# Kernel optimization log

Hardware: AMD Instinct MI355X
Metric: run time of the kernel (lower is better)

The kernel has to match this reference:

```python
import jax, jax.numpy as jnp
from jax import lax
import numpy as np

B, C, H, W = 16, 192, 128, 128
NF = 192


def hard_sigmoid(x):
    # Keras 1.x hard_sigmoid: clip(0.2*x + 0.5, 0, 1)
    return jnp.clip(0.2 * x + 0.5, 0.0, 1.0)


def setup_inputs() -> dict:
    key = jax.random.key(0)
    k1, k2, k3 = jax.random.split(key, 3)
    x = jax.random.normal(k1, (B, C, H, W), dtype=jnp.float32)
    W_iof = jax.random.normal(k2, (4 * NF, C, 1, 1), dtype=jnp.float32) * 0.05
    U_iof = jax.random.normal(k3, (4 * NF, NF, 3, 1), dtype=jnp.float32) * 0.05
    b_iof = jnp.zeros((4 * NF,), dtype=jnp.float32)
    init_h = jnp.zeros((NF, W), dtype=jnp.float32)
    init_c = jnp.zeros((NF, W), dtype=jnp.float32)
    return {"x": x, "W_iof": W_iof, "U_iof": U_iof, "b_iof": b_iof,
            "init_h": init_h, "init_c": init_c}


def reference(x, W_iof, U_iof, b_iof, init_h, init_c):
    b, c, h_dim, w_dim = x.shape
    nf = init_h.shape[0]
    in3 = c // 3
    out3 = nf // 3
    # pyramid channel mask on the 1x1 input-to-state weights
    mask = jnp.ones((4 * nf, c), dtype=x.dtype)
    mask = mask.at[:out3, in3:].set(0.0)
    mask = mask.at[out3:2 * out3, 2 * in3:].set(0.0)
    Wm = W_iof[:, :, 0, 0] * mask  # (4nf, c)
    U = U_iof[:, :, :, 0]          # (4nf, nf, 3)

    # direction 'Down': scan over rows (H). Precompute input-to-state for all rows.
    X = jnp.transpose(x, (0, 2, 1, 3))  # (B, H, C, W)
    i2s = jnp.einsum('bhcw,oc->bhow', X, Wm) + b_iof[None, None, :, None]  # (B,H,4nf,W)

    h0 = jnp.broadcast_to(init_h[None], (b, nf, w_dim))
    c0 = jnp.broadcast_to(init_c[None], (b, nf, w_dim))

    def step(carry, its):
        h_tm1, c_tm1 = carry
        # 3-wide cross-correlation along W, 'half' padding (lax conv is correlation)
        s2s = lax.conv_general_dilated(h_tm1, U, (1,), [(1, 1)],
                                       dimension_numbers=('NCH', 'OIH', 'NCH'))
        gates = its + s2s  # (B, 4nf, W)
        ofi = hard_sigmoid(gates[:, :3 * nf])
        o = ofi[:, :nf]
        f = ofi[:, nf:2 * nf]
        i = ofi[:, 2 * nf:3 * nf]
        g = jnp.tanh(gates[:, 3 * nf:])
        c_new = f * c_tm1 + i * g
        h_new = o * jnp.tanh(c_new)
        return (h_new, c_new), h_new

    _, hs = lax.scan(step, (h0, c0), jnp.transpose(i2s, (1, 0, 2, 3)))  # (H,B,nf,W)
    # return_sequences=True then permute (0,2,1,3): (B, H, nf, W) -> (B, nf, H, W)
    return jnp.transpose(hs, (1, 2, 0, 3))
```

## Files before the change

kernel.cpp:

```cpp
#include <hip/hip_runtime.h>
#include <math.h>

#define BB 16
#define CC 192
#define NF 192
#define HH 128
#define WW 128
#define G4 768
#define KTOT 768
#define LDA 776
#define NJB 12
#define GRIDSZ (NJB * BB)
#define SMEM_BYTES (64 * LDA * 2)

typedef __bf16 bf16x8 __attribute__((ext_vector_type(8)));
typedef float  f32x4  __attribute__((ext_vector_type(4)));

__device__ unsigned g_cnt[BB * 64];

__device__ __forceinline__ float hsig(float v) {
    float y = fmaf(0.2f, v, 0.5f);
    return fminf(fmaxf(y, 0.f), 1.f);
}

__device__ __forceinline__ float tanh_fast(float x) {
    float y = fminf(fmaxf(x, -8.f), 8.f) * 2.885390082f;
    float e = __builtin_amdgcn_exp2f(y);
    float r = __builtin_amdgcn_rcpf(e + 1.f);
    return fmaf(-2.f, r, 1.f);
}

__device__ __forceinline__ unsigned short f2bf(float f) {
    unsigned int u = __float_as_uint(f);
    u += 0x7fffu + ((u >> 16) & 1u);
    return (unsigned short)(u >> 16);
}

__global__ void prep_weights(const float* __restrict__ Wf,
                             const float* __restrict__ Uf,
                             unsigned short* __restrict__ Wc) {
    int idx = blockIdx.x * blockDim.x + threadIdx.x;
    if (idx < BB)
        g_cnt[idx * 64] = 0u;
    if (idx >= G4 * KTOT) return;
    int row = idx / KTOT;
    int k   = idx - row * KTOT;
    float v;
    if (k < CC) {
        int lim = row < 64 ? 64 : (row < 128 ? 128 : 192);
        v = (k < lim) ? Wf[row * CC + k] : 0.f;
    } else {
        int kp = k - CC;
        int d  = kp / CC;
        int c  = kp - d * CC;
        v = Uf[((size_t)row * CC + c) * 3 + d];
    }
    Wc[idx] = f2bf(v);
}

__global__ void prep_bx(const float* __restrict__ x, unsigned short* __restrict__ Bsrc) {
    int idx = blockIdx.x * blockDim.x + threadIdx.x;
    if (idx >= HH * BB * WW) return;
    int w = idx & (WW - 1);
    int r = idx >> 7;
    int b = r & (BB - 1);
    int t = r >> 4;
    const float* xp = x + ((size_t)b * CC * HH + t) * WW + w;
    unsigned short* dp = Bsrc + (size_t)idx * KTOT;
#pragma unroll
    for (int cc = 0; cc < CC / 8; ++cc) {
        unsigned short v[8];
#pragma unroll
        for (int i = 0; i < 8; ++i)
            v[i] = f2bf(xp[(size_t)(cc * 8 + i) * (HH * WW)]);
        *(uint4*)(dp + cc * 8) = *(uint4*)v;
    }
}

__global__ void prep_bh_oob(unsigned short* __restrict__ Bsrc) {
    int idx = blockIdx.x * blockDim.x + threadIdx.x;
    if (idx >= HH * BB * 384) return;
    int u = idx % 384;
    int r = idx / 384;
    int b = r & (BB - 1);
    int t = r >> 4;
    size_t base = ((size_t)(t * BB + b) * WW) * KTOT;
    size_t off = (u < 192) ? (size_t)0 * KTOT + 192 + u
                           : (size_t)127 * KTOT + 384 + u;
    Bsrc[base + off] = 0;
}

__global__ void prep_bh0(const float* __restrict__ init_h, unsigned short* __restrict__ Bsrc) {
    int idx = blockIdx.x * blockDim.x + threadIdx.x;
    if (idx >= BB * WW * 576) return;
    int kp = idx % 576;
    int r  = idx / 576;
    int w  = r & (WW - 1);
    int b  = r >> 7;
    int d  = kp / CC;
    int c  = kp - d * CC;
    int wt = w + d - 1;
    float v = (wt >= 0 && wt < WW) ? init_h[c * WW + wt] : 0.f;
    Bsrc[((size_t)b * WW + w) * KTOT + CC + kp] = f2bf(v);
}

__global__ __launch_bounds__(512, 1) void lstm_persist(
    const unsigned short* __restrict__ Wc,
    unsigned short* __restrict__ Bsrc,
    const float* __restrict__ bias,
    const float* __restrict__ init_c,
    float* __restrict__ out)
{
    extern __shared__ unsigned short smem[];
    unsigned short (*Alds)[LDA] = (unsigned short(*)[LDA])smem;

    const int tid  = threadIdx.x;
    const int nw   = tid >> 6;
    const int lane = tid & 63;
    const int m    = lane & 15;
    const int q    = lane >> 4;
    const int jb   = blockIdx.x % NJB;
    const int b    = blockIdx.x / NJB;
    const int j0   = jb * 16;
    const int w    = nw * 16 + m;
    unsigned* const cntp = &g_cnt[b * 64];

    for (int u = tid; u < 64 * 96; u += 512) {
        int r  = u / 96;
        int ko = (u - r * 96) * 8;
        int grow = (r >> 4) * NF + j0 + (r & 15);
        *(uint4*)&Alds[r][ko] = *(const uint4*)(Wc + (size_t)grow * KTOT + ko);
    }
    float breg[4][4];
#pragma unroll
    for (int g = 0; g < 4; ++g)
#pragma unroll
        for (int r = 0; r < 4; ++r)
            breg[g][r] = bias[g * NF + j0 + q * 4 + r];
    float creg[4];
#pragma unroll
    for (int r = 0; r < 4; ++r)
        creg[r] = init_c[(j0 + q * 4 + r) * WW + w];
    __syncthreads();

    bf16x8 bxc[6], bxn[6];
    {
        const unsigned short* B0 = Bsrc + ((size_t)b * WW + w) * KTOT;
#pragma unroll
        for (int kc = 0; kc < 6; ++kc)
            bxc[kc] = *(const bf16x8*)(B0 + kc * 32 + q * 8);
    }

    for (int t = 0; t < HH; ++t) {
        f32x4 acc[4];
#pragma unroll
        for (int g = 0; g < 4; ++g)
            acc[g] = (f32x4){breg[g][0], breg[g][1], breg[g][2], breg[g][3]};

        const unsigned short* Bn =
            Bsrc + ((size_t)(t * BB + b) * WW + w) * KTOT;

#pragma unroll
        for (int kc = 0; kc < 6; ++kc) {
            const int k = kc * 32 + q * 8;
            bf16x8 a0 = *(const bf16x8*)&Alds[ 0 + m][k];
            bf16x8 a1 = *(const bf16x8*)&Alds[16 + m][k];
            bf16x8 a2 = *(const bf16x8*)&Alds[32 + m][k];
            bf16x8 a3 = *(const bf16x8*)&Alds[48 + m][k];
            acc[0] = __builtin_amdgcn_mfma_f32_16x16x32_bf16(a0, bxc[kc], acc[0], 0, 0, 0);
            acc[1] = __builtin_amdgcn_mfma_f32_16x16x32_bf16(a1, bxc[kc], acc[1], 0, 0, 0);
            acc[2] = __builtin_amdgcn_mfma_f32_16x16x32_bf16(a2, bxc[kc], acc[2], 0, 0, 0);
            acc[3] = __builtin_amdgcn_mfma_f32_16x16x32_bf16(a3, bxc[kc], acc[3], 0, 0, 0);
        }

        if (t > 0) {
            const unsigned need = (unsigned)(NJB * t);
            while (__hip_atomic_load(cntp, __ATOMIC_RELAXED,
                                     __HIP_MEMORY_SCOPE_AGENT) < need)
                __builtin_amdgcn_s_sleep(1);
            __builtin_amdgcn_fence(__ATOMIC_ACQUIRE, "workgroup");
        }

        bf16x8 bh[18];
#pragma unroll
        for (int kc = 0; kc < 18; ++kc)
            bh[kc] = *(const bf16x8*)(Bn + 192 + kc * 32 + q * 8);

        if (t < HH - 1) {
            const unsigned short* Bx = Bn + (size_t)BB * WW * KTOT;
#pragma unroll
            for (int kc = 0; kc < 6; ++kc)
                bxn[kc] = *(const bf16x8*)(Bx + kc * 32 + q * 8);
        }

#pragma unroll
        for (int kc = 0; kc < 18; ++kc) {
            const int k = 192 + kc * 32 + q * 8;
            bf16x8 a0 = *(const bf16x8*)&Alds[ 0 + m][k];
            bf16x8 a1 = *(const bf16x8*)&Alds[16 + m][k];
            bf16x8 a2 = *(const bf16x8*)&Alds[32 + m][k];
            bf16x8 a3 = *(const bf16x8*)&Alds[48 + m][k];
            acc[0] = __builtin_amdgcn_mfma_f32_16x16x32_bf16(a0, bh[kc], acc[0], 0, 0, 0);
            acc[1] = __builtin_amdgcn_mfma_f32_16x16x32_bf16(a1, bh[kc], acc[1], 0, 0, 0);
            acc[2] = __builtin_amdgcn_mfma_f32_16x16x32_bf16(a2, bh[kc], acc[2], 0, 0, 0);
            acc[3] = __builtin_amdgcn_mfma_f32_16x16x32_bf16(a3, bh[kc], acc[3], 0, 0, 0);
        }

        float hn[4];
#pragma unroll
        for (int r = 0; r < 4; ++r) {
            float og = hsig(acc[0][r]);
            float fg = hsig(acc[1][r]);
            float ig = hsig(acc[2][r]);
            float gg = tanh_fast(acc[3][r]);
            float cn = fmaf(fg, creg[r], ig * gg);
            creg[r] = cn;
            hn[r] = og * tanh_fast(cn);
        }

        if (t < HH - 1) {
            unsigned long long pk =
                  (unsigned long long)f2bf(hn[0])
                | ((unsigned long long)f2bf(hn[1]) << 16)
                | ((unsigned long long)f2bf(hn[2]) << 32)
                | ((unsigned long long)f2bf(hn[3]) << 48);
            unsigned short* Bns =
                Bsrc + ((size_t)((t + 1) * BB + b) * WW) * KTOT;
            const int jo = CC + j0 + q * 4;
            __hip_atomic_store((unsigned long long*)
                (Bns + (size_t)w * KTOT + jo + CC), pk,
                __ATOMIC_RELAXED, __HIP_MEMORY_SCOPE_AGENT);
            if (w < WW - 1)
                __hip_atomic_store((unsigned long long*)
                    (Bns + (size_t)(w + 1) * KTOT + jo), pk,
                    __ATOMIC_RELAXED, __HIP_MEMORY_SCOPE_AGENT);
            if (w > 0)
                __hip_atomic_store((unsigned long long*)
                    (Bns + (size_t)(w - 1) * KTOT + jo + 2 * CC), pk,
                    __ATOMIC_RELAXED, __HIP_MEMORY_SCOPE_AGENT);
            asm volatile("s_waitcnt vmcnt(0)" ::: "memory");
            __syncthreads();
            if (tid == 0)
                __hip_atomic_fetch_add(cntp, 1u, __ATOMIC_RELAXED,
                                       __HIP_MEMORY_SCOPE_AGENT);
        }

#pragma unroll
        for (int r = 0; r < 4; ++r)
            out[(((size_t)b * NF + j0 + q * 4 + r) * HH + t) * WW + w] = hn[r];

#pragma unroll
        for (int kc = 0; kc < 6; ++kc)
            bxc[kc] = bxn[kc];
    }
}

extern "C" void kernel_launch(void* const* d_in, const int* in_sizes, int n_in,
                              void* d_out, int out_size, void* d_ws, size_t ws_size,
                              hipStream_t stream) {
    const float* x      = (const float*)d_in[0];
    const float* W_iof  = (const float*)d_in[1];
    const float* U_iof  = (const float*)d_in[2];
    const float* b_iof  = (const float*)d_in[3];
    const float* init_h = (const float*)d_in[4];
    const float* init_c = (const float*)d_in[5];
    float* out = (float*)d_out;

    unsigned short* Wc   = (unsigned short*)d_ws;
    unsigned short* Bsrc = Wc + (size_t)G4 * KTOT;

    prep_weights<<<(G4 * KTOT + 255) / 256, 256, 0, stream>>>(W_iof, U_iof, Wc);
    prep_bx<<<(HH * BB * WW + 255) / 256, 256, 0, stream>>>(x, Bsrc);
    prep_bh_oob<<<(HH * BB * 384 + 255) / 256, 256, 0, stream>>>(Bsrc);
    prep_bh0<<<(BB * WW * 576 + 255) / 256, 256, 0, stream>>>(init_h, Bsrc);

    const unsigned short* Wcp = Wc;
    unsigned short* Bsp = Bsrc;
    const float* bp = b_iof;
    const float* icp = init_c;
    float* op = out;
    void* args[] = {&Wcp, &Bsp, &bp, &icp, &op};
    hipLaunchCooperativeKernel((const void*)lstm_persist, dim3(GRIDSZ), dim3(512),
                               args, SMEM_BYTES, stream);
}
```

Before: 1.459 ms.

## Switch to 32x32x16 MFMA with split-K across two wave groups and LDS reduction

```diff
diff --git a/kernel.cpp b/kernel.cpp
--- a/kernel.cpp
+++ b/kernel.cpp
@@ -11,10 +11,12 @@
 #define LDA 776
 #define NJB 12
 #define GRIDSZ (NJB * BB)
-#define SMEM_BYTES (64 * LDA * 2)
+#define RED_STRIDE 36
+#define SMEM_BYTES (64 * LDA * 2 + 4 * 64 * RED_STRIDE * 4)
 
 typedef __bf16 bf16x8 __attribute__((ext_vector_type(8)));
 typedef float  f32x4  __attribute__((ext_vector_type(4)));
+typedef float  f32x16 __attribute__((ext_vector_type(16)));
 
 __device__ unsigned g_cnt[BB * 64];
 
@@ -113,16 +115,19 @@
 {
     extern __shared__ unsigned short smem[];
     unsigned short (*Alds)[LDA] = (unsigned short(*)[LDA])smem;
+    float* red = (float*)(smem + 64 * LDA);
 
     const int tid  = threadIdx.x;
     const int nw   = tid >> 6;
     const int lane = tid & 63;
-    const int m    = lane & 15;
-    const int q    = lane >> 4;
+    const int c31  = lane & 31;
+    const int l5   = lane >> 5;
+    const bool grp0 = (nw < 4);
+    const int ws   = grp0 ? nw : nw - 4;
+    const int w    = ws * 32 + c31;
     const int jb   = blockIdx.x % NJB;
     const int b    = blockIdx.x / NJB;
     const int j0   = jb * 16;
-    const int w    = nw * 16 + m;
     unsigned* const cntp = &g_cnt[b * 64];
 
     for (int u = tid; u < 64 * 96; u += 512) {
@@ -131,46 +136,55 @@
         int grow = (r >> 4) * NF + j0 + (r & 15);
         *(uint4*)&Alds[r][ko] = *(const uint4*)(Wc + (size_t)grow * KTOT + ko);
     }
-    float breg[4][4];
-#pragma unroll
-    for (int g = 0; g < 4; ++g)
-#pragma unroll
-        for (int r = 0; r < 4; ++r)
-            breg[g][r] = bias[g * NF + j0 + q * 4 + r];
-    float creg[4];
-#pragma unroll
-    for (int r = 0; r < 4; ++r)
-        creg[r] = init_c[(j0 + q * 4 + r) * WW + w];
+
+    float biasr[4][8];
+    float creg[8];
+    if (grp0) {
+#pragma unroll
+        for (int r = 0; r < 8; ++r) {
+            const int jq = (r & 3) + 8 * (r >> 2) + 4 * l5;
+#pragma unroll
+            for (int g = 0; g < 4; ++g)
+                biasr[g][r] = bias[g * NF + j0 + jq];
+            creg[r] = init_c[(j0 + jq) * WW + w];
+        }
+    }
     __syncthreads();
 
-    bf16x8 bxc[6], bxn[6];
-    {
+    bf16x8 bxc[12], bxn[12];
+    if (grp0) {
         const unsigned short* B0 = Bsrc + ((size_t)b * WW + w) * KTOT;
 #pragma unroll
-        for (int kc = 0; kc < 6; ++kc)
-            bxc[kc] = *(const bf16x8*)(B0 + kc * 32 + q * 8);
-    }
-
+        for (int s = 0; s < 12; ++s)
+            bxc[s] = *(const bf16x8*)(B0 + s * 16 + l5 * 8);
+    }
+
+    float hn[8];
     for (int t = 0; t < HH; ++t) {
-        f32x4 acc[4];
-#pragma unroll
-        for (int g = 0; g < 4; ++g)
-            acc[g] = (f32x4){breg[g][0], breg[g][1], breg[g][2], breg[g][3]};
+        f32x16 acc0, acc1;
+        if (grp0) {
+#pragma unroll
+            for (int r = 0; r < 8; ++r) {
+                acc0[r] = biasr[0][r]; acc0[r + 8] = biasr[1][r];
+                acc1[r] = biasr[2][r]; acc1[r + 8] = biasr[3][r];
+            }
+        } else {
+#pragma unroll
+            for (int i = 0; i < 16; ++i) { acc0[i] = 0.f; acc1[i] = 0.f; }
+        }
 
         const unsigned short* Bn =
             Bsrc + ((size_t)(t * BB + b) * WW + w) * KTOT;
 
-#pragma unroll
-        for (int kc = 0; kc < 6; ++kc) {
-            const int k = kc * 32 + q * 8;
-            bf16x8 a0 = *(const bf16x8*)&Alds[ 0 + m][k];
-            bf16x8 a1 = *(const bf16x8*)&Alds[16 + m][k];
-            bf16x8 a2 = *(const bf16x8*)&Alds[32 + m][k];
-            bf16x8 a3 = *(const bf16x8*)&Alds[48 + m][k];
-            acc[0] = __builtin_amdgcn_mfma_f32_16x16x32_bf16(a0, bxc[kc], acc[0], 0, 0, 0);
-            acc[1] = __builtin_amdgcn_mfma_f32_16x16x32_bf16(a1, bxc[kc], acc[1], 0, 0, 0);
-            acc[2] = __builtin_amdgcn_mfma_f32_16x16x32_bf16(a2, bxc[kc], acc[2], 0, 0, 0);
-            acc[3] = __builtin_amdgcn_mfma_f32_16x16x32_bf16(a3, bxc[kc], acc[3], 0, 0, 0);
+        if (grp0) {
+#pragma unroll
+            for (int s = 0; s < 12; ++s) {
+                const int k = s * 16 + l5 * 8;
+                bf16x8 a0 = *(const bf16x8*)&Alds[c31][k];
+                bf16x8 a1 = *(const bf16x8*)&Alds[32 + c31][k];
+                acc0 = __builtin_amdgcn_mfma_f32_32x32x16_bf16(a0, bxc[s], acc0, 0, 0, 0);
+                acc1 = __builtin_amdgcn_mfma_f32_32x32x16_bf16(a1, bxc[s], acc1, 0, 0, 0);
+            }
         }
 
         if (t > 0) {
@@ -181,77 +195,130 @@
             __builtin_amdgcn_fence(__ATOMIC_ACQUIRE, "workgroup");
         }
 
-        bf16x8 bh[18];
-#pragma unroll
-        for (int kc = 0; kc < 18; ++kc)
-            bh[kc] = *(const bf16x8*)(Bn + 192 + kc * 32 + q * 8);
+        if (grp0) {
+            bf16x8 bd[12];
+#pragma unroll
+            for (int s = 0; s < 12; ++s)
+                bd[s] = *(const bf16x8*)(Bn + 192 + s * 16 + l5 * 8);
+            if (t < HH - 1) {
+                const unsigned short* Bx = Bn + (size_t)BB * WW * KTOT;
+#pragma unroll
+                for (int s = 0; s < 12; ++s)
+                    bxn[s] = *(const bf16x8*)(Bx + s * 16 + l5 * 8);
+            }
+#pragma unroll
+            for (int s = 0; s < 12; ++s) {
+                const int k = (12 + s) * 16 + l5 * 8;
+                bf16x8 a0 = *(const bf16x8*)&Alds[c31][k];
+                bf16x8 a1 = *(const bf16x8*)&Alds[32 + c31][k];
+                acc0 = __builtin_amdgcn_mfma_f32_32x32x16_bf16(a0, bd[s], acc0, 0, 0, 0);
+                acc1 = __builtin_amdgcn_mfma_f32_32x32x16_bf16(a1, bd[s], acc1, 0, 0, 0);
+            }
+        } else {
+            bf16x8 bh[24];
+#pragma unroll
+            for (int s = 0; s < 24; ++s)
+                bh[s] = *(const bf16x8*)(Bn + 384 + s * 16 + l5 * 8);
+#pragma unroll
+            for (int s = 0; s < 24; ++s) {
+                const int k = (24 + s) * 16 + l5 * 8;
+                bf16x8 a0 = *(const bf16x8*)&Alds[c31][k];
+                bf16x8 a1 = *(const bf16x8*)&Alds[32 + c31][k];
+                acc0 = __builtin_amdgcn_mfma_f32_32x32x16_bf16(a0, bh[s], acc0, 0, 0, 0);
+                acc1 = __builtin_amdgcn_mfma_f32_32x32x16_bf16(a1, bh[s], acc1, 0, 0, 0);
+            }
+            float* rp = red + (size_t)(ws * 64 + lane) * RED_STRIDE;
+#pragma unroll
+            for (int rb = 0; rb < 4; ++rb) {
+                f32x4 v0 = {acc0[4 * rb], acc0[4 * rb + 1], acc0[4 * rb + 2], acc0[4 * rb + 3]};
+                f32x4 v1 = {acc1[4 * rb], acc1[4 * rb + 1], acc1[4 * rb + 2], acc1[4 * rb + 3]};
+                *(f32x4*)(rp + 4 * rb)      = v0;
+                *(f32x4*)(rp + 16 + 4 * rb) = v1;
+            }
+        }
+        __syncthreads();
+
+        if (grp0) {
+            const float* rp = red + (size_t)(ws * 64 + lane) * RED_STRIDE;
+#pragma unroll
+            for (int rb = 0; rb < 4; ++rb) {
+                f32x4 v0 = *(const f32x4*)(rp + 4 * rb);
+                f32x4 v1 = *(const f32x4*)(rp + 16 + 4 * rb);
+#pragma unroll
+                for (int i = 0; i < 4; ++i) {
+                    acc0[4 * rb + i] += v0[i];
+                    acc1[4 * rb + i] += v1[i];
+                }
+            }
+#pragma unroll
+            for (int r = 0; r < 8; ++r) {
+                float og = hsig(acc0[r]);
+                float fg = hsig(acc0[r + 8]);
+                float ig = hsig(acc1[r]);
+                float gg = tanh_fast(acc1[r + 8]);
+                float cn = fmaf(fg, creg[r], ig * gg);
+                creg[r] = cn;
+                hn[r] = og * tanh_fast(cn);
+            }
+            if (t < HH - 1) {
+                unsigned long long pk0 =
+                      (unsigned long long)f2bf(hn[0])
+                    | ((unsigned long long)f2bf(hn[1]) << 16)
+                    | ((unsigned long long)f2bf(hn[2]) << 32)
+                    | ((unsigned long long)f2bf(hn[3]) << 48);
+                unsigned long long pk1 =
+                      (unsigned long long)f2bf(hn[4])
+                    | ((unsigned long long)f2bf(hn[5]) << 16)
+                    | ((unsigned long long)f2bf(hn[6]) << 32)
+                    | ((unsigned long long)f2bf(hn[7]) << 48);
+                unsigned short* Bns =
+                    Bsrc + ((size_t)((t + 1) * BB + b) * WW) * KTOT;
+                const int joA = CC + j0 + 4 * l5;
+                const int joB = joA + 8;
+                __hip_atomic_store((unsigned long long*)
+                    (Bns + (size_t)w * KTOT + joA + CC), pk0,
+                    __ATOMIC_RELAXED, __HIP_MEMORY_SCOPE_AGENT);
+                __hip_atomic_store((unsigned long long*)
+                    (Bns + (size_t)w * KTOT + joB + CC), pk1,
+                    __ATOMIC_RELAXED, __HIP_MEMORY_SCOPE_AGENT);
+                if (w < WW - 1) {
+                    __hip_atomic_store((unsigned long long*)
+                        (Bns + (size_t)(w + 1) * KTOT + joA), pk0,
+                        __ATOMIC_RELAXED, __HIP_MEMORY_SCOPE_AGENT);
+                    __hip_atomic_store((unsigned long long*)
+                        (Bns + (size_t)(w + 1) * KTOT + joB), pk1,
+                        __ATOMIC_RELAXED, __HIP_MEMORY_SCOPE_AGENT);
+                }
+                if (w > 0) {
+                    __hip_atomic_store((unsigned long long*)
+                        (Bns + (size_t)(w - 1) * KTOT + joA + 2 * CC), pk0,
+                        __ATOMIC_RELAXED, __HIP_MEMORY_SCOPE_AGENT);
+                    __hip_atomic_store((unsigned long long*)
+                        (Bns + (size_t)(w - 1) * KTOT + joB + 2 * CC), pk1,
+                        __ATOMIC_RELAXED, __HIP_MEMORY_SCOPE_AGENT);
+                }
+            }
+        }
 
         if (t < HH - 1) {
-            const unsigned short* Bx = Bn + (size_t)BB * WW * KTOT;
-#pragma unroll
-            for (int kc = 0; kc < 6; ++kc)
-                bxn[kc] = *(const bf16x8*)(Bx + kc * 32 + q * 8);
-        }
-
-#pragma unroll
-        for (int kc = 0; kc < 18; ++kc) {
-            const int k = 192 + kc * 32 + q * 8;
-            bf16x8 a0 = *(const bf16x8*)&Alds[ 0 + m][k];
-            bf16x8 a1 = *(const bf16x8*)&Alds[16 + m][k];
-            bf16x8 a2 = *(const bf16x8*)&Alds[32 + m][k];
-            bf16x8 a3 = *(const bf16x8*)&Alds[48 + m][k];
-            acc[0] = __builtin_amdgcn_mfma_f32_16x16x32_bf16(a0, bh[kc], acc[0], 0, 0, 0);
-            acc[1] = __builtin_amdgcn_mfma_f32_16x16x32_bf16(a1, bh[kc], acc[1], 0, 0, 0);
-            acc[2] = __builtin_amdgcn_mfma_f32_16x16x32_bf16(a2, bh[kc], acc[2], 0, 0, 0);
-            acc[3] = __builtin_amdgcn_mfma_f32_16x16x32_bf16(a3, bh[kc], acc[3], 0, 0, 0);
-        }
-
-        float hn[4];
-#pragma unroll
-        for (int r = 0; r < 4; ++r) {
-            float og = hsig(acc[0][r]);
-            float fg = hsig(acc[1][r]);
-            float ig = hsig(acc[2][r]);
-            float gg = tanh_fast(acc[3][r]);
-            float cn = fmaf(fg, creg[r], ig * gg);
-            creg[r] = cn;
-            hn[r] = og * tanh_fast(cn);
-        }
-
-        if (t < HH - 1) {
-            unsigned long long pk =
-                  (unsigned long long)f2bf(hn[0])
-                | ((unsigned long long)f2bf(hn[1]) << 16)
-                | ((unsigned long long)f2bf(hn[2]) << 32)
-                | ((unsigned long long)f2bf(hn[3]) << 48);
-            unsigned short* Bns =
-                Bsrc + ((size_t)((t + 1) * BB + b) * WW) * KTOT;
-            const int jo = CC + j0 + q * 4;
-            __hip_atomic_store((unsigned long long*)
-                (Bns + (size_t)w * KTOT + jo + CC), pk,
-                __ATOMIC_RELAXED, __HIP_MEMORY_SCOPE_AGENT);
-            if (w < WW - 1)
-                __hip_atomic_store((unsigned long long*)
-                    (Bns + (size_t)(w + 1) * KTOT + jo), pk,
-                    __ATOMIC_RELAXED, __HIP_MEMORY_SCOPE_AGENT);
-            if (w > 0)
-                __hip_atomic_store((unsigned long long*)
-                    (Bns + (size_t)(w - 1) * KTOT + jo + 2 * CC), pk,
-                    __ATOMIC_RELAXED, __HIP_MEMORY_SCOPE_AGENT);
-            asm volatile("s_waitcnt vmcnt(0)" ::: "memory");
+            if (grp0)
+                asm volatile("s_waitcnt vmcnt(0)" ::: "memory");
             __syncthreads();
             if (tid == 0)
                 __hip_atomic_fetch_add(cntp, 1u, __ATOMIC_RELAXED,
                                        __HIP_MEMORY_SCOPE_AGENT);
         }
 
-#pragma unroll
-        for (int r = 0; r < 4; ++r)
-            out[(((size_t)b * NF + j0 + q * 4 + r) * HH + t) * WW + w] = hn[r];
-
-#pragma unroll
-        for (int kc = 0; kc < 6; ++kc)
-            bxc[kc] = bxn[kc];
+        if (grp0) {
+#pragma unroll
+            for (int r = 0; r < 8; ++r) {
+                const int jq = (r & 3) + 8 * (r >> 2) + 4 * l5;
+                out[(((size_t)b * NF + j0 + jq) * HH + t) * WW + w] = hn[r];
+            }
+#pragma unroll
+            for (int s = 0; s < 12; ++s)
+                bxc[s] = bxn[s];
+        }
     }
 }
 
```

Measured after the change: 1.874 ms. +28.4%, slower.
